# Kernel tuning notes

Hardware: AMD Instinct MI355X
Metric: run time of the kernel (lower is better)

Reference implementation:

```python
import jax, jax.numpy as jnp
import numpy as np

N_NODES = 10000
N_EDGES = 160000
D = 128        # embedding_dim = in/out channels
E_DIM = 32     # edge feature dim
HEADS = 3
N_ETYPES = 64
ROUNDS = 2     # num_message_rounds
NEG_SLOPE = 0.2


def _lookup_maxnorm(table, idx):
    # torch Embedding(max_norm=1): rows with L2 norm > 1 are renormalized to norm 1
    v = table[idx]
    n = jnp.linalg.norm(v, axis=-1, keepdims=True)
    return v / jnp.maximum(n, 1.0)


def _edge_gat(x, src, dst, edge_attr, weight, att, euw, bias):
    # x: [N, D]; src/dst: [E] (self loops included); edge_attr: [E, E_DIM]
    N = x.shape[0]
    H = HEADS
    C = weight.shape[1] // H
    xh = (x @ weight).reshape(N, H, C)                 # [N, H, C]
    x_j = xh[src]                                      # gather source nodes  [E, H, C]
    x_i = xh[dst]                                      # gather target nodes  [E, H, C]
    ea = jnp.broadcast_to(edge_attr[:, None, :], (src.shape[0], H, edge_attr.shape[-1]))
    xj_cat = jnp.concatenate([x_j, ea], axis=-1)       # [E, H, C+E_DIM]
    # attention logits: (cat(x_i, x_j, e) * att).sum(-1)
    alpha = jnp.sum(jnp.concatenate([x_i, xj_cat], axis=-1) * att, axis=-1)  # [E, H]
    alpha = jax.nn.leaky_relu(alpha, NEG_SLOPE)
    # scatter-softmax over incoming edges of each dst node (stable)
    m = jax.ops.segment_max(alpha, dst, num_segments=N)        # [N, H]
    a = jnp.exp(alpha - m[dst])
    denom = jax.ops.segment_sum(a, dst, num_segments=N)        # [N, H]
    a = a / denom[dst]
    # weighted scatter-add aggregate
    aggr = jax.ops.segment_sum(xj_cat * a[..., None], dst, num_segments=N)  # [N, H, C+E_DIM]
    return aggr.mean(axis=1) @ euw + bias                       # [N, C]


def setup_inputs() -> dict:
    key = jax.random.key(0)
    ks = jax.random.split(key, 13)
    x_idx = jnp.arange(N_NODES, dtype=jnp.int32)
    src = jax.random.randint(ks[0], (N_EDGES,), 0, N_NODES, dtype=jnp.int32)
    off = jax.random.randint(ks[1], (N_EDGES,), 1, N_NODES, dtype=jnp.int32)
    dst = (src + off) % N_NODES    # guaranteed self-loop-free
    edge_index = jnp.stack([src, dst])
    edge_attr_idx = jax.random.randint(ks[2], (N_EDGES,), 0, N_ETYPES, dtype=jnp.int32)
    def g(k, shape):
        return jax.random.normal(k, shape, jnp.float32) * np.float32(np.sqrt(2.0 / sum(shape)))
    node_emb = g(ks[3], (N_NODES, D))
    edge_emb = g(ks[4], (N_ETYPES, E_DIM))
    w1 = g(ks[5], (D, HEADS * D))
    att1 = g(ks[6], (1, HEADS, 2 * D + E_DIM))
    euw1 = g(ks[7], (D + E_DIM, D))
    b1 = jnp.zeros((D,), jnp.float32)
    w2 = g(ks[8], (D, HEADS * D))
    att2 = g(ks[9], (1, HEADS, 2 * D + E_DIM))
    euw2 = g(ks[10], (D + E_DIM, D))
    b2 = jnp.zeros((D,), jnp.float32)
    return dict(x_idx=x_idx, edge_index=edge_index, edge_attr_idx=edge_attr_idx,
                node_emb=node_emb, edge_emb=edge_emb,
                w1=w1, att1=att1, euw1=euw1, b1=b1,
                w2=w2, att2=att2, euw2=euw2, b2=b2)


def reference(x_idx, edge_index, edge_attr_idx, node_emb, edge_emb,
              w1, att1, euw1, b1, w2, att2, euw2, b2):
    N = node_emb.shape[0]
    src0, dst0 = edge_index[0], edge_index[1]
    loop = jnp.arange(N, dtype=src0.dtype)
    src = jnp.concatenate([src0, loop])
    dst = jnp.concatenate([dst0, loop])
    x = _lookup_maxnorm(node_emb, x_idx)               # [N, D]
    ea = edge_emb[edge_attr_idx]                       # [E0, E_DIM]
    ea_full = jnp.concatenate([ea, jnp.zeros((N, ea.shape[-1]), ea.dtype)], axis=0)
    for _ in range(ROUNDS):
        # eval mode: dropout is identity
        x = jax.nn.elu(_edge_gat(x, src, dst, ea_full, w1, att1, euw1, b1))
        x = _edge_gat(x, src, dst, ea_full, w2, att2, euw2, b2)
    return x
```

## Files before the change

kernel.cpp:

```cpp
#include <hip/hip_runtime.h>
#include <hip/hip_bf16.h>

typedef __hip_bfloat16 bf16;
typedef __attribute__((ext_vector_type(8))) short short8;
typedef __attribute__((ext_vector_type(4))) float f32x4;
typedef __attribute__((ext_vector_type(4), aligned(4))) int i32x4u;
typedef __attribute__((ext_vector_type(4))) int i32x4;

__device__ __forceinline__ float b2f(bf16 v) { return __bfloat162float(v); }
__device__ __forceinline__ float2 i2f2(int w) {
  float lo = __uint_as_float(((unsigned)w) << 16);
  float hi = __uint_as_float(((unsigned)w) & 0xFFFF0000u);
  return make_float2(lo, hi);
}
__device__ __forceinline__ unsigned f2bfb(float f) {
  unsigned u = __float_as_uint(f);
  unsigned r = 0x7FFFu + ((u >> 16) & 1u);
  return (u + r) >> 16;
}
__device__ __forceinline__ unsigned pk2(float a, float b) {
  return f2bfb(a) | (f2bfb(b) << 16);
}
__device__ __forceinline__ float ldv(const void* p, int i, int f) {
  return f ? ((const float*)p)[i] : b2f(((const bf16*)p)[i]);
}

#define SH 392

__global__ __launch_bounds__(256) void wconv_kernel(
    const void* __restrict__ ee, const void* __restrict__ w1,
    const void* __restrict__ a1, const void* __restrict__ eu1,
    const void* __restrict__ b1, const void* __restrict__ w2,
    const void* __restrict__ a2, const void* __restrict__ eu2,
    const void* __restrict__ b2, int* __restrict__ flag,
    float* __restrict__ eef, float* __restrict__ att1f, float* __restrict__ att2f,
    float* __restrict__ b1f, float* __restrict__ b2f,
    bf16* __restrict__ WT1, bf16* __restrict__ WT2,
    bf16* __restrict__ euT1, bf16* __restrict__ euT2,
    float* __restrict__ s_et, int* __restrict__ counts, int N) {
  __shared__ int cnt;
  __shared__ int fl;
  if (threadIdx.x == 0) cnt = 0;
  __syncthreads();
  const unsigned short* probe = (const unsigned short*)w1;
  int local = 0;
#pragma unroll
  for (int k = 0; k < 8; ++k) {
    int e = (probe[threadIdx.x * 8 + k] >> 7) & 0xFF;
    if (e >= 160) local++;
  }
  if (local) atomicAdd(&cnt, local);
  __syncthreads();
  if (threadIdx.x == 0) {
    fl = (cnt > 16) ? 1 : 0;
    if (blockIdx.x == 0) *flag = fl;
  }
  __syncthreads();
  int f = fl;

  int i = blockIdx.x * 256 + threadIdx.x;
  if (i < 2048) {
    eef[i] = ldv(ee, i, f);
  } else if (i < 2912) {
    att1f[i - 2048] = ldv(a1, i - 2048, f);
  } else if (i < 3776) {
    att2f[i - 2912] = ldv(a2, i - 2912, f);
  } else if (i < 3904) {
    b1f[i - 3776] = ldv(b1, i - 3776, f);
  } else if (i < 4032) {
    b2f[i - 3904] = ldv(b2, i - 3904, f);
  } else if (i < 53184) {
    int j = i - 4032; int c = j >> 7, k = j & 127;
    WT1[j] = __float2bfloat16(ldv(w1, k * 384 + c, f));
  } else if (i < 102336) {
    int j = i - 53184; int c = j >> 7, k = j & 127;
    WT2[j] = __float2bfloat16(ldv(w2, k * 384 + c, f));
  } else if (i < 122816) {
    int j = i - 102336; int c = j / 160, k = j % 160;
    euT1[j] = __float2bfloat16(ldv(eu1, k * 128 + c, f));
  } else if (i < 143296) {
    int j = i - 122816; int c = j / 160, k = j % 160;
    euT2[j] = __float2bfloat16(ldv(eu2, k * 128 + c, f));
  } else if (i < 143296 + N) {
    counts[i - 143296] = 0;
  }

  if (blockIdx.x == 0) {
    for (int id = threadIdx.x; id < 2 * 65 * 3; id += 256) {
      int l = id / (65 * 3);
      int r = id % (65 * 3);
      int t = r / 3, h = r % 3;
      const void* att = l ? a2 : a1;
      float s = 0.0f;
      if (t < 64) {
        for (int d = 0; d < 32; ++d)
          s += ldv(ee, t * 32 + d, f) * ldv(att, h * 288 + 256 + d, f);
      }
      s_et[id] = s;
    }
  }
}

__global__ __launch_bounds__(256) void prep_kernel(
    const int* __restrict__ x_idx, const void* __restrict__ node_emb,
    const int* __restrict__ flag, bf16* __restrict__ xb,
    int* __restrict__ counts, const int* __restrict__ dst, int E0, int N) {
  int wid = threadIdx.x >> 6, lane = threadIdx.x & 63;
  int n = blockIdx.x * 4 + wid;
  if (n < N) {
    int idx = x_idx[n];
    if ((unsigned)idx >= (unsigned)N) idx = 0;
    float v0, v1;
    if (*flag) {
      const float* er = (const float*)node_emb + (size_t)idx * 128;
      v0 = er[lane]; v1 = er[lane + 64];
    } else {
      const bf16* er = (const bf16*)node_emb + (size_t)idx * 128;
      v0 = b2f(er[lane]); v1 = b2f(er[lane + 64]);
    }
    float ss = v0 * v0 + v1 * v1;
#pragma unroll
    for (int d = 32; d > 0; d >>= 1) ss += __shfl_xor(ss, d);
    float norm = sqrtf(ss);
    float scale = norm > 1.0f ? 1.0f / norm : 1.0f;
    xb[(size_t)n * 128 + lane] = __float2bfloat16(v0 * scale);
    xb[(size_t)n * 128 + 64 + lane] = __float2bfloat16(v1 * scale);
  }
  int gid = blockIdx.x * 256 + threadIdx.x;
  int stride = gridDim.x * 256;
  for (int i = gid; i < E0; i += stride) {
    int d = dst[i];
    if ((unsigned)d >= (unsigned)N) d = 0;
    atomicAdd(&counts[d], 1);
  }
}

__global__ __launch_bounds__(1024) void scan_kernel(
    int* __restrict__ counts, int* __restrict__ row_ptr, int N) {
  __shared__ int wsum[16];
  int t = threadIdx.x;
  int chunk = (N + 1023) >> 10;
  int lo = t * chunk;
  int hi = lo + chunk;
  if (lo > N) lo = N;
  if (hi > N) hi = N;
  int s = 0;
  for (int i = lo; i < hi; ++i) s += counts[i] + 1;
  int lane = t & 63, wv = t >> 6;
  int incl = s;
#pragma unroll
  for (int d = 1; d < 64; d <<= 1) {
    int u = __shfl_up(incl, d);
    if (lane >= d) incl += u;
  }
  if (lane == 63) wsum[wv] = incl;
  __syncthreads();
  if (t == 0) {
    int run = 0;
#pragma unroll
    for (int w = 0; w < 16; ++w) { int c = wsum[w]; wsum[w] = run; run += c; }
  }
  __syncthreads();
  int run = incl - s + wsum[wv];
  for (int i = lo; i < hi; ++i) {
    int c = counts[i] + 1;
    row_ptr[i] = run;
    counts[i] = run;
    run += c;
  }
  if (t == 1023) row_ptr[N] = run;
}

__global__ __launch_bounds__(256) void scatter_kernel(
    const int* __restrict__ src, const int* __restrict__ dst,
    const int* __restrict__ et, int* __restrict__ cursor,
    int* __restrict__ packed, int E0, int N) {
  int E = E0 + N;
  int i = blockIdx.x * blockDim.x + threadIdx.x;
  if (i < E0) {
    int d = dst[i];
    if ((unsigned)d >= (unsigned)N) d = 0;
    int p = atomicAdd(&cursor[d], 1);
    if ((unsigned)p >= (unsigned)E) p = 0;
    int t = et[i] & 63;
    packed[p] = (src[i] & 0xFFFF) | (t << 16);
  } else if (i < E) {
    int n = i - E0;
    int p = atomicAdd(&cursor[n], 1);
    if ((unsigned)p >= (unsigned)E) p = 0;
    packed[p] = (n & 0xFFFF) | (64 << 16);
  }
}

__global__ __launch_bounds__(384) void gemm_xh_s_mfma(
    const bf16* __restrict__ x, const bf16* __restrict__ WT,
    const float* __restrict__ attf, bf16* __restrict__ xh,
    float* __restrict__ s_i, float* __restrict__ s_j, int N) {
  __shared__ bf16 stage[32 * SH];
  __shared__ float lds_i[6][32];
  __shared__ float lds_j[6][32];
  int wave = threadIdx.x >> 6, lane = threadIdx.x & 63;
  int row_base = blockIdx.x * 32;
  int quad = lane >> 4, r16 = lane & 15;
  int rowA = row_base + r16;      if (rowA >= N) rowA = N - 1;
  int rowB = row_base + 16 + r16; if (rowB >= N) rowB = N - 1;
  const short8* apA = (const short8*)(x + (size_t)rowA * 128 + quad * 8);
  const short8* apB = (const short8*)(x + (size_t)rowB * 128 + quad * 8);
  short8 aA[4], aB[4];
#pragma unroll
  for (int kk = 0; kk < 4; ++kk) { aA[kk] = apA[kk * 4]; aB[kk] = apB[kk * 4]; }

  float piA[4] = {0.f, 0.f, 0.f, 0.f}, pjA[4] = {0.f, 0.f, 0.f, 0.f};
  float piB[4] = {0.f, 0.f, 0.f, 0.f}, pjB[4] = {0.f, 0.f, 0.f, 0.f};
#pragma unroll
  for (int j = 0; j < 4; ++j) {
    int col = wave * 64 + j * 16 + r16;
    const short8* bp = (const short8*)(WT + (size_t)col * 128 + quad * 8);
    short8 b[4];
#pragma unroll
    for (int kk = 0; kk < 4; ++kk) b[kk] = bp[kk * 4];
    f32x4 accA = {0.f, 0.f, 0.f, 0.f};
    f32x4 accB = {0.f, 0.f, 0.f, 0.f};
#pragma unroll
    for (int kk = 0; kk < 4; ++kk) {
      accA = __builtin_amdgcn_mfma_f32_16x16x32_bf16(aA[kk], b[kk], accA, 0, 0, 0);
      accB = __builtin_amdgcn_mfma_f32_16x16x32_bf16(aB[kk], b[kk], accB, 0, 0, 0);
    }
    int h = col >> 7, fi = col & 127, pair = fi >> 1, sub = fi & 1;
    int base = pair * 6 + h * 2 + sub;
#pragma unroll
    for (int r = 0; r < 4; ++r) {
      stage[(quad * 4 + r) * SH + base] = __float2bfloat16(accA[r]);
      stage[(16 + quad * 4 + r) * SH + base] = __float2bfloat16(accB[r]);
    }
    float ai = attf[h * 288 + fi];
    float aj = attf[h * 288 + 128 + fi];
#pragma unroll
    for (int r = 0; r < 4; ++r) {
      piA[r] = fmaf(accA[r], ai, piA[r]);
      pjA[r] = fmaf(accA[r], aj, pjA[r]);
      piB[r] = fmaf(accB[r], ai, piB[r]);
      pjB[r] = fmaf(accB[r], aj, pjB[r]);
    }
  }
#pragma unroll
  for (int d = 1; d < 16; d <<= 1) {
#pragma unroll
    for (int r = 0; r < 4; ++r) {
      piA[r] += __shfl_xor(piA[r], d);
      pjA[r] += __shfl_xor(pjA[r], d);
      piB[r] += __shfl_xor(piB[r], d);
      pjB[r] += __shfl_xor(pjB[r], d);
    }
  }
  if (r16 == 0) {
#pragma unroll
    for (int r = 0; r < 4; ++r) {
      lds_i[wave][quad * 4 + r] = piA[r];
      lds_j[wave][quad * 4 + r] = pjA[r];
      lds_i[wave][16 + quad * 4 + r] = piB[r];
      lds_j[wave][16 + quad * 4 + r] = pjB[r];
    }
  }
  __syncthreads();
  int m = threadIdx.x;
  if (m < 96) {
    int h = m / 32, r = m % 32;
    int node = row_base + r;
    if (node < N) s_i[node * 3 + h] = lds_i[2 * h][r] + lds_i[2 * h + 1][r];
  } else if (m < 192) {
    int tt = m - 96;
    int h = tt / 32, r = tt % 32;
    int node = row_base + r;
    if (node < N) s_j[node * 3 + h] = lds_j[2 * h][r] + lds_j[2 * h + 1][r];
  }
#pragma unroll
  for (int k = 0; k < 4; ++k) {
    int c = threadIdx.x + k * 384;
    int r = c / 48, o = c % 48;
    int node = row_base + r;
    if (node < N)
      *(i32x4*)(xh + (size_t)node * 384 + o * 8) =
          *(const i32x4*)(stage + r * SH + o * 8);
  }
}

__global__ __launch_bounds__(384) void fox_kernel(
    const bf16* __restrict__ aggr, const bf16* __restrict__ euwT,
    const float* __restrict__ biasf, int do_elu,
    const bf16* __restrict__ WT, const float* __restrict__ attf,
    bf16* __restrict__ xh, float* __restrict__ s_i, float* __restrict__ s_j,
    int N) {
  __shared__ bf16 xtile[16][136];
  __shared__ bf16 stage[16 * SH];
  __shared__ float lds_i[6][16];
  __shared__ float lds_j[6][16];
  int wave = threadIdx.x >> 6, lane = threadIdx.x & 63;
  int quad = lane >> 4, r16 = lane & 15;
  int row_base = blockIdx.x * 16;
  int row = row_base + r16; if (row >= N) row = N - 1;

  const short8* ap = (const short8*)(aggr + (size_t)row * 160 + quad * 8);
  short8 aa[5];
#pragma unroll
  for (int kk = 0; kk < 5; ++kk) aa[kk] = ap[kk * 4];
  for (int t = wave; t < 8; t += 6) {
    int col = t * 16 + r16;
    const short8* bp = (const short8*)(euwT + (size_t)col * 160 + quad * 8);
    f32x4 acc = {0.f, 0.f, 0.f, 0.f};
#pragma unroll
    for (int kk = 0; kk < 5; ++kk)
      acc = __builtin_amdgcn_mfma_f32_16x16x32_bf16(aa[kk], bp[kk * 4], acc, 0, 0, 0);
    float bv = biasf[col];
#pragma unroll
    for (int r = 0; r < 4; ++r) {
      float v = acc[r] + bv;
      if (do_elu) v = v > 0.0f ? v : expm1f(v);
      xtile[quad * 4 + r][col] = __float2bfloat16(v);
    }
  }
  __syncthreads();

  short8 a[4];
#pragma unroll
  for (int kk = 0; kk < 4; ++kk)
    a[kk] = *(const short8*)(&xtile[r16][quad * 8 + kk * 32]);

  float pi_r[4] = {0.f, 0.f, 0.f, 0.f};
  float pj_r[4] = {0.f, 0.f, 0.f, 0.f};
#pragma unroll
  for (int j = 0; j < 4; ++j) {
    int col = wave * 64 + j * 16 + r16;
    const short8* bp = (const short8*)(WT + (size_t)col * 128 + quad * 8);
    f32x4 acc = {0.f, 0.f, 0.f, 0.f};
#pragma unroll
    for (int kk = 0; kk < 4; ++kk)
      acc = __builtin_amdgcn_mfma_f32_16x16x32_bf16(a[kk], bp[kk * 4], acc, 0, 0, 0);
    int h = col >> 7, fi = col & 127, pair = fi >> 1, sub = fi & 1;
    int base = pair * 6 + h * 2 + sub;
#pragma unroll
    for (int r = 0; r < 4; ++r)
      stage[(quad * 4 + r) * SH + base] = __float2bfloat16(acc[r]);
    float ai = attf[h * 288 + fi];
    float aj = attf[h * 288 + 128 + fi];
#pragma unroll
    for (int r = 0; r < 4; ++r) {
      pi_r[r] = fmaf(acc[r], ai, pi_r[r]);
      pj_r[r] = fmaf(acc[r], aj, pj_r[r]);
    }
  }
#pragma unroll
  for (int d = 1; d < 16; d <<= 1) {
#pragma unroll
    for (int r = 0; r < 4; ++r) {
      pi_r[r] += __shfl_xor(pi_r[r], d);
      pj_r[r] += __shfl_xor(pj_r[r], d);
    }
  }
  if (r16 == 0) {
#pragma unroll
    for (int r = 0; r < 4; ++r) {
      lds_i[wave][quad * 4 + r] = pi_r[r];
      lds_j[wave][quad * 4 + r] = pj_r[r];
    }
  }
  __syncthreads();
  int m = threadIdx.x;
  if (m < 48) {
    int h = m / 16, r = m % 16;
    int node = row_base + r;
    if (node < N) s_i[node * 3 + h] = lds_i[2 * h][r] + lds_i[2 * h + 1][r];
  } else if (m < 96) {
    int tt = m - 48;
    int h = tt / 16, r = tt % 16;
    int node = row_base + r;
    if (node < N) s_j[node * 3 + h] = lds_j[2 * h][r] + lds_j[2 * h + 1][r];
  }
#pragma unroll
  for (int k = 0; k < 2; ++k) {
    int c = threadIdx.x + k * 384;
    int r = c / 48, o = c % 48;
    int node = row_base + r;
    if (node < N)
      *(i32x4*)(xh + (size_t)node * 384 + o * 8) =
          *(const i32x4*)(stage + r * SH + o * 8);
  }
}

__global__ __launch_bounds__(256) void edge_aggr_kernel(
    const int* __restrict__ xh_i, const float* __restrict__ s_i,
    const float* __restrict__ s_j, const float* __restrict__ s_et,
    const float2* __restrict__ eef2, const int* __restrict__ row_ptr,
    const int* __restrict__ packed, unsigned* __restrict__ aggr_u,
    int N, int E) {
  __shared__ float lds[2][512];
  int wid = threadIdx.x >> 6, lane = threadIdx.x & 63;
  int nodeLocal = wid >> 1, w = wid & 1;
  int n0 = blockIdx.x * 2 + nodeLocal;
  int n = n0 < N ? n0 : N - 1;
  int start = row_ptr[n], end = row_ptr[n + 1];
  if (start < 0) start = 0;
  if (start > E) start = E;
  if (end < start) end = start;
  if (end > E) end = E;
  int deg = end - start;
  float si0 = s_i[n * 3 + 0], si1 = s_i[n * 3 + 1], si2 = s_i[n * 3 + 2];

  float p0r = 0.f, p1r = 0.f, p2r = 0.f;
  int pkr = 0;
  float dp0 = 0.0f, dp1 = 0.0f, dp2 = 0.0f;
  int slot = 2 * lane + w;
  if (slot < deg) {
    int p = packed[start + slot];
    int s = p & 0xFFFF; if (s >= N) s = N - 1;
    int t = (p >> 16) & 127; if (t > 64) t = 64;
    float a0 = si0 + s_j[s * 3 + 0] + s_et[t * 3 + 0];
    float a1 = si1 + s_j[s * 3 + 1] + s_et[t * 3 + 1];
    float a2 = si2 + s_j[s * 3 + 2] + s_et[t * 3 + 2];
    a0 = a0 > 0.0f ? a0 : 0.2f * a0;
    a1 = a1 > 0.0f ? a1 : 0.2f * a1;
    a2 = a2 > 0.0f ? a2 : 0.2f * a2;
    a0 = fminf(fmaxf(a0, -60.0f), 60.0f);
    a1 = fminf(fmaxf(a1, -60.0f), 60.0f);
    a2 = fminf(fmaxf(a2, -60.0f), 60.0f);
    p0r = __expf(a0); p1r = __expf(a1); p2r = __expf(a2);
    dp0 = p0r; dp1 = p1r; dp2 = p2r;
    pkr = s | (t << 16);
  }
#pragma unroll
  for (int d = 32; d > 0; d >>= 1) {
    dp0 += __shfl_xor(dp0, d);
    dp1 += __shfl_xor(dp1, d);
    dp2 += __shfl_xor(dp2, d);
  }
  float d0 = dp0, d1 = dp1, d2 = dp2;

  float2 ax0 = make_float2(0.f, 0.f), ax1 = ax0, ax2 = ax0;
  float2 ae0 = ax0, ae1 = ax0, ae2 = ax0;
  int capped = deg < 128 ? deg : 128;
  int cnt = (capped > w) ? ((capped - w + 1) >> 1) : 0;

  {
    int j = 0;
    for (; j + 2 <= cnt; j += 2) {
      int pkA = __shfl(pkr, j), pkB = __shfl(pkr, j + 1);
      float qA0 = __shfl(p0r, j), qB0 = __shfl(p0r, j + 1);
      float qA1 = __shfl(p1r, j), qB1 = __shfl(p1r, j + 1);
      float qA2 = __shfl(p2r, j), qB2 = __shfl(p2r, j + 1);
      int sA = pkA & 0xFFFF, tA = pkA >> 16;
      int sB = pkB & 0xFFFF, tB = pkB >> 16;
      i32x4u qA = *(const i32x4u*)(xh_i + (size_t)sA * 192 + lane * 3);
      i32x4u qB = *(const i32x4u*)(xh_i + (size_t)sB * 192 + lane * 3);
      float2 vA0 = i2f2(qA.x), vA1 = i2f2(qA.y), vA2 = i2f2(qA.z);
      float2 vB0 = i2f2(qB.x), vB1 = i2f2(qB.y), vB2 = i2f2(qB.z);
      ax0.x = fmaf(qA0, vA0.x, ax0.x); ax0.y = fmaf(qA0, vA0.y, ax0.y);
      ax1.x = fmaf(qA1, vA1.x, ax1.x); ax1.y = fmaf(qA1, vA1.y, ax1.y);
      ax2.x = fmaf(qA2, vA2.x, ax2.x); ax2.y = fmaf(qA2, vA2.y, ax2.y);
      ax0.x = fmaf(qB0, vB0.x, ax0.x); ax0.y = fmaf(qB0, vB0.y, ax0.y);
      ax1.x = fmaf(qB1, vB1.x, ax1.x); ax1.y = fmaf(qB1, vB1.y, ax1.y);
      ax2.x = fmaf(qB2, vB2.x, ax2.x); ax2.y = fmaf(qB2, vB2.y, ax2.y);
      if (lane < 16) {
        if (tA != 64) {
          float2 ev = eef2[tA * 16 + lane];
          ae0.x = fmaf(qA0, ev.x, ae0.x); ae0.y = fmaf(qA0, ev.y, ae0.y);
          ae1.x = fmaf(qA1, ev.x, ae1.x); ae1.y = fmaf(qA1, ev.y, ae1.y);
          ae2.x = fmaf(qA2, ev.x, ae2.x); ae2.y = fmaf(qA2, ev.y, ae2.y);
        }
        if (tB != 64) {
          float2 ev = eef2[tB * 16 + lane];
          ae0.x = fmaf(qB0, ev.x, ae0.x); ae0.y = fmaf(qB0, ev.y, ae0.y);
          ae1.x = fmaf(qB1, ev.x, ae1.x); ae1.y = fmaf(qB1, ev.y, ae1.y);
          ae2.x = fmaf(qB2, ev.x, ae2.x); ae2.y = fmaf(qB2, ev.y, ae2.y);
        }
      }
    }
    if (j < cnt) {
      int pkA = __shfl(pkr, j);
      float qA0 = __shfl(p0r, j), qA1 = __shfl(p1r, j), qA2 = __shfl(p2r, j);
      int sA = pkA & 0xFFFF, tA = pkA >> 16;
      i32x4u qA = *(const i32x4u*)(xh_i + (size_t)sA * 192 + lane * 3);
      float2 vA0 = i2f2(qA.x), vA1 = i2f2(qA.y), vA2 = i2f2(qA.z);
      ax0.x = fmaf(qA0, vA0.x, ax0.x); ax0.y = fmaf(qA0, vA0.y, ax0.y);
      ax1.x = fmaf(qA1, vA1.x, ax1.x); ax1.y = fmaf(qA1, vA1.y, ax1.y);
      ax2.x = fmaf(qA2, vA2.x, ax2.x); ax2.y = fmaf(qA2, vA2.y, ax2.y);
      if (lane < 16 && tA != 64) {
        float2 ev = eef2[tA * 16 + lane];
        ae0.x = fmaf(qA0, ev.x, ae0.x); ae0.y = fmaf(qA0, ev.y, ae0.y);
        ae1.x = fmaf(qA1, ev.x, ae1.x); ae1.y = fmaf(qA1, ev.y, ae1.y);
        ae2.x = fmaf(qA2, ev.x, ae2.x); ae2.y = fmaf(qA2, ev.y, ae2.y);
      }
    }
  }

  if (w == 0) {
    for (int e = start + 128; e < end; ++e) {
      int p = packed[e];
      int s = p & 0xFFFF; if (s >= N) s = N - 1;
      int t = (p >> 16) & 127; if (t > 64) t = 64;
      float a0 = si0 + s_j[s * 3 + 0] + s_et[t * 3 + 0];
      float a1 = si1 + s_j[s * 3 + 1] + s_et[t * 3 + 1];
      float a2 = si2 + s_j[s * 3 + 2] + s_et[t * 3 + 2];
      a0 = a0 > 0.0f ? a0 : 0.2f * a0;
      a1 = a1 > 0.0f ? a1 : 0.2f * a1;
      a2 = a2 > 0.0f ? a2 : 0.2f * a2;
      a0 = fminf(fmaxf(a0, -60.0f), 60.0f);
      a1 = fminf(fmaxf(a1, -60.0f), 60.0f);
      a2 = fminf(fmaxf(a2, -60.0f), 60.0f);
      float p0 = __expf(a0), p1 = __expf(a1), p2 = __expf(a2);
      d0 += p0; d1 += p1; d2 += p2;
      i32x4u q = *(const i32x4u*)(xh_i + (size_t)s * 192 + lane * 3);
      float2 v0 = i2f2(q.x), v1 = i2f2(q.y), v2 = i2f2(q.z);
      ax0.x = fmaf(p0, v0.x, ax0.x); ax0.y = fmaf(p0, v0.y, ax0.y);
      ax1.x = fmaf(p1, v1.x, ax1.x); ax1.y = fmaf(p1, v1.y, ax1.y);
      ax2.x = fmaf(p2, v2.x, ax2.x); ax2.y = fmaf(p2, v2.y, ax2.y);
      if (t != 64 && lane < 16) {
        float2 ev = eef2[t * 16 + lane];
        ae0.x = fmaf(p0, ev.x, ae0.x); ae0.y = fmaf(p0, ev.y, ae0.y);
        ae1.x = fmaf(p1, ev.x, ae1.x); ae1.y = fmaf(p1, ev.y, ae1.y);
        ae2.x = fmaf(p2, ev.x, ae2.x); ae2.y = fmaf(p2, ev.y, ae2.y);
      }
    }
  }

  float* L = lds[nodeLocal];
  if (w == 1) {
    L[lane * 2 + 0] = ax0.x;       L[lane * 2 + 1] = ax0.y;
    L[128 + lane * 2 + 0] = ax1.x; L[128 + lane * 2 + 1] = ax1.y;
    L[256 + lane * 2 + 0] = ax2.x; L[256 + lane * 2 + 1] = ax2.y;
    if (lane < 16) {
      L[384 + lane * 2 + 0] = ae0.x; L[384 + lane * 2 + 1] = ae0.y;
      L[416 + lane * 2 + 0] = ae1.x; L[416 + lane * 2 + 1] = ae1.y;
      L[448 + lane * 2 + 0] = ae2.x; L[448 + lane * 2 + 1] = ae2.y;
    }
    if (lane == 0) { L[480] = d0; L[481] = d1; L[482] = d2; }
  }
  __syncthreads();
  if (w == 0 && n0 < N) {
    ax0.x += L[lane * 2 + 0];       ax0.y += L[lane * 2 + 1];
    ax1.x += L[128 + lane * 2 + 0]; ax1.y += L[128 + lane * 2 + 1];
    ax2.x += L[256 + lane * 2 + 0]; ax2.y += L[256 + lane * 2 + 1];
    if (lane < 16) {
      ae0.x += L[384 + lane * 2 + 0]; ae0.y += L[384 + lane * 2 + 1];
      ae1.x += L[416 + lane * 2 + 0]; ae1.y += L[416 + lane * 2 + 1];
      ae2.x += L[448 + lane * 2 + 0]; ae2.y += L[448 + lane * 2 + 1];
    }
    d0 += L[480]; d1 += L[481]; d2 += L[482];
    const float third = 1.0f / 3.0f;
    float i0 = third / fmaxf(d0, 1e-30f);
    float i1 = third / fmaxf(d1, 1e-30f);
    float i2 = third / fmaxf(d2, 1e-30f);
    aggr_u[(size_t)n0 * 80 + lane] =
        pk2(ax0.x * i0 + ax1.x * i1 + ax2.x * i2,
            ax0.y * i0 + ax1.y * i1 + ax2.y * i2);
    if (lane < 16)
      aggr_u[(size_t)n0 * 80 + 64 + lane] =
          pk2(ae0.x * i0 + ae1.x * i1 + ae2.x * i2,
              ae0.y * i0 + ae1.y * i1 + ae2.y * i2);
  }
}

__global__ __launch_bounds__(256) void gemm_out_mfma(
    const bf16* __restrict__ aggr, const bf16* __restrict__ euwT,
    const float* __restrict__ biasf, void* __restrict__ dout,
    const int* __restrict__ flag, int N) {
  int wave = threadIdx.x >> 6, lane = threadIdx.x & 63;
  int row_base = blockIdx.x * 16;
  int col_base = blockIdx.y * 64 + wave * 16;
  int quad = lane >> 4, r16 = lane & 15;
  int row = row_base + r16; if (row >= N) row = N - 1;
  int col = col_base + r16;
  f32x4 acc = {0.f, 0.f, 0.f, 0.f};
  const short8* ap = (const short8*)(aggr + (size_t)row * 160 + quad * 8);
  const short8* bp = (const short8*)(euwT + (size_t)col * 160 + quad * 8);
#pragma unroll
  for (int kk = 0; kk < 5; ++kk) {
    short8 a = ap[kk * 4];
    short8 b = bp[kk * 4];
    acc = __builtin_amdgcn_mfma_f32_16x16x32_bf16(a, b, acc, 0, 0, 0);
  }
  float bv = biasf[col];
  int f = *flag;
#pragma unroll
  for (int r = 0; r < 4; ++r) {
    int node = row_base + quad * 4 + r;
    if (node < N) {
      float v = acc[r] + bv;
      if (f) ((float*)dout)[(size_t)node * 128 + col] = v;
      else   ((bf16*)dout)[(size_t)node * 128 + col] = __float2bfloat16(v);
    }
  }
}

extern "C" void kernel_launch(void* const* d_in, const int* in_sizes, int n_in,
                              void* d_out, int out_size, void* d_ws, size_t ws_size,
                              hipStream_t stream) {
  const int* x_idx = (const int*)d_in[0];
  const int* edge_index = (const int*)d_in[1];
  const int* edge_attr_idx = (const int*)d_in[2];

  int N = in_sizes[0];
  int E0 = in_sizes[1] / 2;
  int E = E0 + N;
  const int* src = edge_index;
  const int* dst = edge_index + E0;

  size_t off = 0;
  char* base = (char*)d_ws;
  auto carve = [&](size_t bytes) -> void* {
    void* p = base + off;
    off += (bytes + 255) & ~(size_t)255;
    return p;
  };
  int* flag     = (int*)carve(256);
  int* counts   = (int*)carve((size_t)N * 4);
  int* row_ptr  = (int*)carve((size_t)(N + 1) * 4);
  int* packed   = (int*)carve((size_t)E * 4);
  float* s_i    = (float*)carve((size_t)N * 3 * 4);
  float* s_j    = (float*)carve((size_t)N * 3 * 4);
  float* s_et   = (float*)carve(2 * 65 * 3 * 4);
  float* eef    = (float*)carve(2048 * 4);
  float* att1f  = (float*)carve(864 * 4);
  float* att2f  = (float*)carve(864 * 4);
  float* b1f    = (float*)carve(128 * 4);
  float* b2f_   = (float*)carve(128 * 4);
  bf16* WT1     = (bf16*)carve(49152 * 2);
  bf16* WT2     = (bf16*)carve(49152 * 2);
  bf16* euT1    = (bf16*)carve(20480 * 2);
  bf16* euT2    = (bf16*)carve(20480 * 2);
  bf16* xh      = (bf16*)carve((size_t)N * 384 * 2 + 64);
  bf16* aggr    = (bf16*)carve((size_t)N * 160 * 2);
  bf16* xb      = (bf16*)d_out;
  (void)n_in; (void)out_size; (void)ws_size;

  wconv_kernel<<<(143296 + N + 255) / 256, 256, 0, stream>>>(
      d_in[4], d_in[5], d_in[6], d_in[7], d_in[8], d_in[9], d_in[10], d_in[11],
      d_in[12], flag, eef, att1f, att2f, b1f, b2f_, WT1, WT2, euT1, euT2,
      s_et, counts, N);
  int nb4 = (N + 3) / 4;
  prep_kernel<<<nb4, 256, 0, stream>>>(x_idx, d_in[3], flag, xb, counts, dst,
                                       E0, N);
  scan_kernel<<<1, 1024, 0, stream>>>(counts, row_ptr, N);
  scatter_kernel<<<(E + 255) / 256, 256, 0, stream>>>(src, dst, edge_attr_idx,
                                                      counts, packed, E0, N);

  int nrb16 = (N + 15) / 16;
  int nrb32 = (N + 31) / 32;
  int nb2 = (N + 1) / 2;

  gemm_xh_s_mfma<<<nrb32, 384, 0, stream>>>(xb, WT1, att1f, xh, s_i, s_j, N);
  edge_aggr_kernel<<<nb2, 256, 0, stream>>>(
      (const int*)xh, s_i, s_j, s_et, (const float2*)eef,
      row_ptr, packed, (unsigned*)aggr, N, E);
  fox_kernel<<<nrb16, 384, 0, stream>>>(aggr, euT1, b1f, 1, WT2, att2f,
                                        xh, s_i, s_j, N);
  edge_aggr_kernel<<<nb2, 256, 0, stream>>>(
      (const int*)xh, s_i, s_j, s_et + 195, (const float2*)eef,
      row_ptr, packed, (unsigned*)aggr, N, E);
  fox_kernel<<<nrb16, 384, 0, stream>>>(aggr, euT2, b2f_, 0, WT1, att1f,
                                        xh, s_i, s_j, N);
  edge_aggr_kernel<<<nb2, 256, 0, stream>>>(
      (const int*)xh, s_i, s_j, s_et, (const float2*)eef,
      row_ptr, packed, (unsigned*)aggr, N, E);
  fox_kernel<<<nrb16, 384, 0, stream>>>(aggr, euT1, b1f, 1, WT2, att2f,
                                        xh, s_i, s_j, N);
  edge_aggr_kernel<<<nb2, 256, 0, stream>>>(
      (const int*)xh, s_i, s_j, s_et + 195, (const float2*)eef,
      row_ptr, packed, (unsigned*)aggr, N, E);
  gemm_out_mfma<<<dim3(nrb16, 2), 256, 0, stream>>>(aggr, euT2, b2f_,
                                                    d_out, flag, N);
}
```

Before: 315.3 us.

## Pad interleaved xh rows to 512 bf16 for aligned 16-byte gathers, unroll edge loop by 4

Each node's projected features are stored interleaved as pairs of 3 heads padded to 4 ints per lane, so the row stride becomes 512 bf16. The per-edge gather in the aggregation kernel can then use naturally aligned 16-byte vector loads instead of unaligned 12-byte ones. The edge loop is also unrolled from 2 to 4 to keep more gathers in flight. The cost is a third more bytes written and read for xh per edge, plus more register pressure.

```diff
diff --git a/kernel.cpp b/kernel.cpp
--- a/kernel.cpp
+++ b/kernel.cpp
@@ -4,7 +4,6 @@
 typedef __hip_bfloat16 bf16;
 typedef __attribute__((ext_vector_type(8))) short short8;
 typedef __attribute__((ext_vector_type(4))) float f32x4;
-typedef __attribute__((ext_vector_type(4), aligned(4))) int i32x4u;
 typedef __attribute__((ext_vector_type(4))) int i32x4;
 
 __device__ __forceinline__ float b2f(bf16 v) { return __bfloat162float(v); }
@@ -25,7 +24,7 @@
   return f ? ((const float*)p)[i] : b2f(((const bf16*)p)[i]);
 }
 
-#define SH 392
+#define SH 520
 
 __global__ __launch_bounds__(256) void wconv_kernel(
     const void* __restrict__ ee, const void* __restrict__ w1,
@@ -196,7 +195,7 @@
     const bf16* __restrict__ x, const bf16* __restrict__ WT,
     const float* __restrict__ attf, bf16* __restrict__ xh,
     float* __restrict__ s_i, float* __restrict__ s_j, int N) {
-  __shared__ bf16 stage[32 * SH];
+  __shared__ __align__(16) bf16 stage[32 * SH];
   __shared__ float lds_i[6][32];
   __shared__ float lds_j[6][32];
   int wave = threadIdx.x >> 6, lane = threadIdx.x & 63;
@@ -227,7 +226,7 @@
       accB = __builtin_amdgcn_mfma_f32_16x16x32_bf16(aB[kk], b[kk], accB, 0, 0, 0);
     }
     int h = col >> 7, fi = col & 127, pair = fi >> 1, sub = fi & 1;
-    int base = pair * 6 + h * 2 + sub;
+    int base = pair * 8 + h * 2 + sub;
 #pragma unroll
     for (int r = 0; r < 4; ++r) {
       stage[(quad * 4 + r) * SH + base] = __float2bfloat16(accA[r]);
@@ -275,13 +274,15 @@
     if (node < N) s_j[node * 3 + h] = lds_j[2 * h][r] + lds_j[2 * h + 1][r];
   }
 #pragma unroll
-  for (int k = 0; k < 4; ++k) {
+  for (int k = 0; k < 6; ++k) {
     int c = threadIdx.x + k * 384;
-    int r = c / 48, o = c % 48;
-    int node = row_base + r;
-    if (node < N)
-      *(i32x4*)(xh + (size_t)node * 384 + o * 8) =
-          *(const i32x4*)(stage + r * SH + o * 8);
+    if (c < 2048) {
+      int r = c >> 6, o = c & 63;
+      int node = row_base + r;
+      if (node < N)
+        *(i32x4*)(xh + (size_t)node * 512 + o * 8) =
+            *(const i32x4*)(stage + r * SH + o * 8);
+    }
   }
 }
 
@@ -292,7 +293,7 @@
     bf16* __restrict__ xh, float* __restrict__ s_i, float* __restrict__ s_j,
     int N) {
   __shared__ bf16 xtile[16][136];
-  __shared__ bf16 stage[16 * SH];
+  __shared__ __align__(16) bf16 stage[16 * SH];
   __shared__ float lds_i[6][16];
   __shared__ float lds_j[6][16];
   int wave = threadIdx.x >> 6, lane = threadIdx.x & 63;
@@ -337,7 +338,7 @@
     for (int kk = 0; kk < 4; ++kk)
       acc = __builtin_amdgcn_mfma_f32_16x16x32_bf16(a[kk], bp[kk * 4], acc, 0, 0, 0);
     int h = col >> 7, fi = col & 127, pair = fi >> 1, sub = fi & 1;
-    int base = pair * 6 + h * 2 + sub;
+    int base = pair * 8 + h * 2 + sub;
 #pragma unroll
     for (int r = 0; r < 4; ++r)
       stage[(quad * 4 + r) * SH + base] = __float2bfloat16(acc[r]);
@@ -377,13 +378,15 @@
     if (node < N) s_j[node * 3 + h] = lds_j[2 * h][r] + lds_j[2 * h + 1][r];
   }
 #pragma unroll
-  for (int k = 0; k < 2; ++k) {
+  for (int k = 0; k < 3; ++k) {
     int c = threadIdx.x + k * 384;
-    int r = c / 48, o = c % 48;
-    int node = row_base + r;
-    if (node < N)
-      *(i32x4*)(xh + (size_t)node * 384 + o * 8) =
-          *(const i32x4*)(stage + r * SH + o * 8);
+    if (c < 1024) {
+      int r = c >> 6, o = c & 63;
+      int node = row_base + r;
+      if (node < N)
+        *(i32x4*)(xh + (size_t)node * 512 + o * 8) =
+            *(const i32x4*)(stage + r * SH + o * 8);
+    }
   }
 }
 
@@ -442,23 +445,39 @@
 
   {
     int j = 0;
-    for (; j + 2 <= cnt; j += 2) {
+    for (; j + 4 <= cnt; j += 4) {
       int pkA = __shfl(pkr, j), pkB = __shfl(pkr, j + 1);
+      int pkC = __shfl(pkr, j + 2), pkD = __shfl(pkr, j + 3);
       float qA0 = __shfl(p0r, j), qB0 = __shfl(p0r, j + 1);
+      float qC0 = __shfl(p0r, j + 2), qD0 = __shfl(p0r, j + 3);
       float qA1 = __shfl(p1r, j), qB1 = __shfl(p1r, j + 1);
+      float qC1 = __shfl(p1r, j + 2), qD1 = __shfl(p1r, j + 3);
       float qA2 = __shfl(p2r, j), qB2 = __shfl(p2r, j + 1);
+      float qC2 = __shfl(p2r, j + 2), qD2 = __shfl(p2r, j + 3);
       int sA = pkA & 0xFFFF, tA = pkA >> 16;
       int sB = pkB & 0xFFFF, tB = pkB >> 16;
-      i32x4u qA = *(const i32x4u*)(xh_i + (size_t)sA * 192 + lane * 3);
-      i32x4u qB = *(const i32x4u*)(xh_i + (size_t)sB * 192 + lane * 3);
+      int sC = pkC & 0xFFFF, tC = pkC >> 16;
+      int sD = pkD & 0xFFFF, tD = pkD >> 16;
+      i32x4 qA = *(const i32x4*)(xh_i + (size_t)sA * 256 + lane * 4);
+      i32x4 qB = *(const i32x4*)(xh_i + (size_t)sB * 256 + lane * 4);
+      i32x4 qC = *(const i32x4*)(xh_i + (size_t)sC * 256 + lane * 4);
+      i32x4 qD = *(const i32x4*)(xh_i + (size_t)sD * 256 + lane * 4);
       float2 vA0 = i2f2(qA.x), vA1 = i2f2(qA.y), vA2 = i2f2(qA.z);
       float2 vB0 = i2f2(qB.x), vB1 = i2f2(qB.y), vB2 = i2f2(qB.z);
+      float2 vC0 = i2f2(qC.x), vC1 = i2f2(qC.y), vC2 = i2f2(qC.z);
+      float2 vD0 = i2f2(qD.x), vD1 = i2f2(qD.y), vD2 = i2f2(qD.z);
       ax0.x = fmaf(qA0, vA0.x, ax0.x); ax0.y = fmaf(qA0, vA0.y, ax0.y);
       ax1.x = fmaf(qA1, vA1.x, ax1.x); ax1.y = fmaf(qA1, vA1.y, ax1.y);
       ax2.x = fmaf(qA2, vA2.x, ax2.x); ax2.y = fmaf(qA2, vA2.y, ax2.y);
       ax0.x = fmaf(qB0, vB0.x, ax0.x); ax0.y = fmaf(qB0, vB0.y, ax0.y);
       ax1.x = fmaf(qB1, vB1.x, ax1.x); ax1.y = fmaf(qB1, vB1.y, ax1.y);
       ax2.x = fmaf(qB2, vB2.x, ax2.x); ax2.y = fmaf(qB2, vB2.y, ax2.y);
+      ax0.x = fmaf(qC0, vC0.x, ax0.x); ax0.y = fmaf(qC0, vC0.y, ax0.y);
+      ax1.x = fmaf(qC1, vC1.x, ax1.x); ax1.y = fmaf(qC1, vC1.y, ax1.y);
+      ax2.x = fmaf(qC2, vC2.x, ax2.x); ax2.y = fmaf(qC2, vC2.y, ax2.y);
+      ax0.x = fmaf(qD0, vD0.x, ax0.x); ax0.y = fmaf(qD0, vD0.y, ax0.y);
+      ax1.x = fmaf(qD1, vD1.x, ax1.x); ax1.y = fmaf(qD1, vD1.y, ax1.y);
+      ax2.x = fmaf(qD2, vD2.x, ax2.x); ax2.y = fmaf(qD2, vD2.y, ax2.y);
       if (lane < 16) {
         if (tA != 64) {
           float2 ev = eef2[tA * 16 + lane];
@@ -472,13 +491,25 @@
           ae1.x = fmaf(qB1, ev.x, ae1.x); ae1.y = fmaf(qB1, ev.y, ae1.y);
           ae2.x = fmaf(qB2, ev.x, ae2.x); ae2.y = fmaf(qB2, ev.y, ae2.y);
         }
+        if (tC != 64) {
+          float2 ev = eef2[tC * 16 + lane];
+          ae0.x = fmaf(qC0, ev.x, ae0.x); ae0.y = fmaf(qC0, ev.y, ae0.y);
+          ae1.x = fmaf(qC1, ev.x, ae1.x); ae1.y = fmaf(qC1, ev.y, ae1.y);
+          ae2.x = fmaf(qC2, ev.x, ae2.x); ae2.y = fmaf(qC2, ev.y, ae2.y);
+        }
+        if (tD != 64) {
+          float2 ev = eef2[tD * 16 + lane];
+          ae0.x = fmaf(qD0, ev.x, ae0.x); ae0.y = fmaf(qD0, ev.y, ae0.y);
+          ae1.x = fmaf(qD1, ev.x, ae1.x); ae1.y = fmaf(qD1, ev.y, ae1.y);
+          ae2.x = fmaf(qD2, ev.x, ae2.x); ae2.y = fmaf(qD2, ev.y, ae2.y);
+        }
       }
     }
-    if (j < cnt) {
+    for (; j < cnt; ++j) {
       int pkA = __shfl(pkr, j);
       float qA0 = __shfl(p0r, j), qA1 = __shfl(p1r, j), qA2 = __shfl(p2r, j);
       int sA = pkA & 0xFFFF, tA = pkA >> 16;
-      i32x4u qA = *(const i32x4u*)(xh_i + (size_t)sA * 192 + lane * 3);
+      i32x4 qA = *(const i32x4*)(xh_i + (size_t)sA * 256 + lane * 4);
       float2 vA0 = i2f2(qA.x), vA1 = i2f2(qA.y), vA2 = i2f2(qA.z);
       ax0.x = fmaf(qA0, vA0.x, ax0.x); ax0.y = fmaf(qA0, vA0.y, ax0.y);
       ax1.x = fmaf(qA1, vA1.x, ax1.x); ax1.y = fmaf(qA1, vA1.y, ax1.y);
@@ -508,7 +539,7 @@
       a2 = fminf(fmaxf(a2, -60.0f), 60.0f);
       float p0 = __expf(a0), p1 = __expf(a1), p2 = __expf(a2);
       d0 += p0; d1 += p1; d2 += p2;
-      i32x4u q = *(const i32x4u*)(xh_i + (size_t)s * 192 + lane * 3);
+      i32x4 q = *(const i32x4*)(xh_i + (size_t)s * 256 + lane * 4);
       float2 v0 = i2f2(q.x), v1 = i2f2(q.y), v2 = i2f2(q.z);
       ax0.x = fmaf(p0, v0.x, ax0.x); ax0.y = fmaf(p0, v0.y, ax0.y);
       ax1.x = fmaf(p1, v1.x, ax1.x); ax1.y = fmaf(p1, v1.y, ax1.y);
@@ -627,7 +658,7 @@
   bf16* WT2     = (bf16*)carve(49152 * 2);
   bf16* euT1    = (bf16*)carve(20480 * 2);
   bf16* euT2    = (bf16*)carve(20480 * 2);
-  bf16* xh      = (bf16*)carve((size_t)N * 384 * 2 + 64);
+  bf16* xh      = (bf16*)carve((size_t)N * 512 * 2 + 64);
   bf16* aggr    = (bf16*)carve((size_t)N * 160 * 2);
   bf16* xb      = (bf16*)d_out;
   (void)n_in; (void)out_size; (void)ws_size;
```

Result: slower. 353.1 us (+12.0%).
